# Kernel optimization log

Measured on AMD Instinct MI355X. Metric: run time of the kernel, lower is better.

The kernel has to match this reference:

```python
import jax, jax.numpy as jnp
import numpy as np

D_MODEL = 1024
NUM_HEADS = 16
DEPTH = D_MODEL // NUM_HEADS
MAX_LEN = 5000


def _make_pe(d_model=D_MODEL, max_len=MAX_LEN):
    # Faithful to torch PositionalEncoding: pe shape [max_len, 1, d_model]
    position = np.arange(max_len, dtype=np.float32)[:, None]
    div_term = np.exp(np.arange(0, d_model, 2, dtype=np.float32) * (-np.log(10000.0) / d_model))
    pe = np.zeros((max_len, d_model), dtype=np.float32)
    pe[:, 0::2] = np.sin(position * div_term)
    pe[:, 1::2] = np.cos(position * div_term)
    return jnp.asarray(pe[:, None, :])  # [max_len, 1, d_model]


def setup_inputs() -> dict:
    key = jax.random.key(0)
    ks = jax.random.split(key, 11)
    B, S, D = 4, 2048, D_MODEL
    s = 1.0 / np.sqrt(D)
    inp = {
        "v": jax.random.normal(ks[0], (B, S, D), jnp.float32),
        "k": jax.random.normal(ks[1], (B, S, D), jnp.float32),
        "q": jax.random.normal(ks[2], (B, S, D), jnp.float32),
        "wq_w": jax.random.normal(ks[3], (D, D), jnp.float32) * s,
        "wq_b": jnp.zeros((D,), jnp.float32),
        "wk_w": jax.random.normal(ks[4], (D, D), jnp.float32) * s,
        "wk_b": jnp.zeros((D,), jnp.float32),
        "wv_w": jax.random.normal(ks[5], (D, D), jnp.float32) * s,
        "wv_b": jnp.zeros((D,), jnp.float32),
        "dense_w": jax.random.normal(ks[6], (D, D), jnp.float32) * s,
        "dense_b": jnp.zeros((D,), jnp.float32),
        "pe": _make_pe(),
    }
    return inp


def _split_heads(x, B):
    # [B, S, D] -> [B, H, S, depth]
    return x.reshape(B, -1, NUM_HEADS, DEPTH).transpose(0, 2, 1, 3)


def reference(v, k, q, wq_w, wq_b, wk_w, wk_b, wv_w, wv_b, dense_w, dense_b, pe):
    B = q.shape[0]
    # Faithful bug-reproduction: pe[:batch] has shape [B, 1, D], broadcast over seq.
    pe_b = pe[:B]  # [B, 1, D]
    q = q + pe_b
    k = k + pe_b
    v = v + pe_b
    # Linear layers (torch: x @ W.T + b)
    qh = _split_heads(q @ wq_w.T + wq_b, B)  # [B,H,Sq,d]
    kh = _split_heads(k @ wk_w.T + wk_b, B)  # [B,H,Sk,d]
    vh = _split_heads(v @ wv_w.T + wv_b, B)  # [B,H,Sk,d]
    scale = 1.0 / jnp.sqrt(jnp.float32(DEPTH))
    logits = jnp.einsum("bhqd,bhkd->bhqk", qh, kh) * scale
    attn = jax.nn.softmax(logits, axis=-1)
    out = jnp.einsum("bhqk,bhkd->bhqd", attn, vh)
    out = out.transpose(0, 2, 1, 3).reshape(B, -1, D_MODEL)
    return out @ dense_w.T + dense_b
```

## Files before the change

### kernel.cpp

```cpp
#include <hip/hip_runtime.h>
#include <hip/hip_bf16.h>

typedef short short8 __attribute__((ext_vector_type(8)));
typedef float f32x4 __attribute__((ext_vector_type(4)));
typedef float f32x16 __attribute__((ext_vector_type(16)));
typedef unsigned int uint4v __attribute__((ext_vector_type(4)));

#define MFMA16(a, b, c) __builtin_amdgcn_mfma_f32_16x16x32_bf16(a, b, c, 0, 0, 0)
#define MFMA32(a, b, c) __builtin_amdgcn_mfma_f32_32x32x16_bf16(a, b, c, 0, 0, 0)

typedef __attribute__((address_space(1))) const unsigned int gas_u32;
typedef __attribute__((address_space(3))) unsigned int las_u32;

__device__ inline void gll16(const void* g, void* l) {
    __builtin_amdgcn_global_load_lds((gas_u32*)g, (las_u32*)l, 16, 0, 0);
}

__device__ inline unsigned short f2bf(float f) {
    unsigned u = __builtin_bit_cast(unsigned, f);
    u += 0x7fff + ((u >> 16) & 1);
    return (unsigned short)(u >> 16);
}

__device__ inline unsigned pk_perm(float a, float b, unsigned sel) {
    unsigned r;
    asm("v_perm_b32 %0, %1, %2, %3"
        : "=v"(r)
        : "v"(__builtin_bit_cast(unsigned, b)), "v"(__builtin_bit_cast(unsigned, a)), "s"(sel));
    return r;
}

__device__ inline float exp2_fast(float x) {
#if __has_builtin(__builtin_amdgcn_exp2f)
    return __builtin_amdgcn_exp2f(x);
#else
    float r; asm("v_exp_f32 %0, %1" : "=v"(r) : "v"(x)); return r;
#endif
}

__device__ inline void pl32_swap(unsigned &a, unsigned &b) {
    asm volatile("v_permlane32_swap_b32 %0, %1" : "+v"(a), "+v"(b));
}

__global__ void pe_cast3(const float* __restrict__ q, const float* __restrict__ k,
                         const float* __restrict__ v, const float* __restrict__ pe,
                         unsigned short* __restrict__ oq, unsigned short* __restrict__ ok,
                         unsigned short* __restrict__ ov) {
    const float* x = (blockIdx.y == 0) ? q : (blockIdx.y == 1) ? k : v;
    unsigned short* o = (blockIdx.y == 0) ? oq : (blockIdx.y == 1) ? ok : ov;
    int i = blockIdx.x * 256 + threadIdx.x;
    long e = (long)i * 4;
    int b = (int)(e >> 21);
    int d = (int)(e & 1023);
    float4 xv = reinterpret_cast<const float4*>(x)[i];
    float4 pv = *reinterpret_cast<const float4*>(pe + b * 1024 + d);
    ushort4 r;
    r.x = f2bf(xv.x + pv.x); r.y = f2bf(xv.y + pv.y);
    r.z = f2bf(xv.z + pv.z); r.w = f2bf(xv.w + pv.w);
    reinterpret_cast<ushort4*>(o)[i] = r;
}

__global__ void wcast4(const float* __restrict__ w0, const float* __restrict__ w1,
                       const float* __restrict__ w2, const float* __restrict__ w3,
                       unsigned short* __restrict__ o0) {
    const float* w = (blockIdx.y == 0) ? w0 : (blockIdx.y == 1) ? w1
                   : (blockIdx.y == 2) ? w2 : w3;
    unsigned short* o = o0 + (size_t)blockIdx.y * 1024 * 1024;
    int i = blockIdx.x * 256 + threadIdx.x;
    float4 xv = reinterpret_cast<const float4*>(w)[i];
    ushort4 r;
    r.x = f2bf(xv.x); r.y = f2bf(xv.y); r.z = f2bf(xv.z); r.w = f2bf(xv.w);
    reinterpret_cast<ushort4*>(o)[i] = r;
}

template <int MODE>
__global__ __launch_bounds__(256, 3) void gemm3(const unsigned short* __restrict__ A0,
                                                const unsigned short* __restrict__ W0,
                                                const float* __restrict__ bq,
                                                const float* __restrict__ bk,
                                                const float* __restrict__ bv,
                                                void* __restrict__ oq,
                                                void* __restrict__ ok,
                                                void* __restrict__ ov,
                                                float qscale) {
    const int NT = 32;
    __shared__ unsigned short lsA[3][128 * 32];
    __shared__ unsigned short lsB[3][128 * 32];

    int z = (MODE == 3) ? blockIdx.z : 0;
    const unsigned short* A = A0 + (size_t)z * 8192 * 1024;
    const unsigned short* W = W0 + (size_t)z * 1024 * 1024;
    const float* bias = (MODE == 3) ? ((z == 0) ? bq : (z == 1) ? bk : bv) : bq;
    float scale = (MODE == 3 && z == 0) ? qscale : 1.0f;

    int tid = threadIdx.x;
    int wave = tid >> 6, lane = tid & 63, lg = lane >> 4, l15 = lane & 15;
    int brow = blockIdx.x * 128;
    int bcol = blockIdx.y * 128;
    int wr = wave >> 1, wc = wave & 1;

    int c0 = wave * 64 + lane, c1 = 256 + c0;
    const unsigned short* sA0 = A + (long)(brow + (c0 >> 2)) * 1024 + ((c0 ^ (c0 >> 2)) & 3) * 8;
    const unsigned short* sA1 = A + (long)(brow + (c1 >> 2)) * 1024 + ((c1 ^ (c1 >> 2)) & 3) * 8;
    const unsigned short* sB0 = W + (long)(bcol + (c0 >> 2)) * 1024 + ((c0 ^ (c0 >> 2)) & 3) * 8;
    const unsigned short* sB1 = W + (long)(bcol + (c1 >> 2)) * 1024 + ((c1 ^ (c1 >> 2)) & 3) * 8;

    int cread = (lg * 16) ^ ((l15 & 3) << 4);

    f32x4 zero4 = {0.f, 0.f, 0.f, 0.f};
    f32x4 acc[4][4];
#pragma unroll
    for (int m = 0; m < 4; ++m)
#pragma unroll
        for (int n = 0; n < 4; ++n) acc[m][n] = zero4;

#define STG(k0, bi) do {                                                  \
        gll16(sA0 + (k0), (char*)lsA[bi] + (wave * 64) * 16);             \
        gll16(sA1 + (k0), (char*)lsA[bi] + (256 + wave * 64) * 16);       \
        gll16(sB0 + (k0), (char*)lsB[bi] + (wave * 64) * 16);             \
        gll16(sB1 + (k0), (char*)lsB[bi] + (256 + wave * 64) * 16);       \
    } while (0)

    STG(0, 0);
    STG(32, 1);

    int bi = 0, sb = 2;
    for (int t = 0; t < NT; ++t) {
        if (t == NT - 1) { asm volatile("s_waitcnt vmcnt(0)" ::: "memory"); }
        else             { asm volatile("s_waitcnt vmcnt(4)" ::: "memory"); }
        __builtin_amdgcn_s_barrier();
        if (t < NT - 2) STG((t + 2) * 32, sb);

        const char* KA = (const char*)lsA[bi];
        const char* KB = (const char*)lsB[bi];
        short8 af[4], bf_[4];
#pragma unroll
        for (int m = 0; m < 4; ++m) {
            int row = wr * 64 + m * 16 + l15;
            af[m] = *(const short8*)(KA + row * 64 + cread);
        }
#pragma unroll
        for (int n = 0; n < 4; ++n) {
            int col = wc * 64 + n * 16 + l15;
            bf_[n] = *(const short8*)(KB + col * 64 + cread);
        }
        __builtin_amdgcn_s_setprio(1);
#pragma unroll
        for (int m = 0; m < 4; ++m)
#pragma unroll
            for (int n = 0; n < 4; ++n) acc[m][n] = MFMA16(af[m], bf_[n], acc[m][n]);
        __builtin_amdgcn_s_setprio(0);

        bi = (bi == 2) ? 0 : bi + 1;
        sb = (sb == 2) ? 0 : sb + 1;
    }
#undef STG

    void* out = (MODE == 3) ? ((z == 0) ? oq : (z == 1) ? ok : ov) : oq;
#pragma unroll
    for (int m = 0; m < 4; ++m)
#pragma unroll
        for (int n = 0; n < 4; ++n) {
            int col = bcol + wc * 64 + n * 16 + l15;
            float bv_ = bias[col];
#pragma unroll
            for (int r = 0; r < 4; ++r) {
                int row = brow + wr * 64 + m * 16 + lg * 4 + r;
                float v = (acc[m][n][r] + bv_) * scale;
                if (MODE == 1) {
                    ((float*)out)[(long)row * 1024 + col] = v;
                } else {
                    int b = row >> 11, s = row & 2047;
                    if (z < 2) {
                        int h = col >> 6, d = col & 63;
                        ((unsigned short*)out)[(((long)(b * 16 + h) * 2048 + s) * 64 + d)] = f2bf(v);
                    } else {
                        ((unsigned short*)out)[((long)(b * 1024 + col)) * 2048 + s] = f2bf(v);
                    }
                }
            }
        }
}

__global__ __launch_bounds__(256, 2) void attn_kernel(const unsigned short* __restrict__ Qh,
                                                      const unsigned short* __restrict__ Kh,
                                                      const unsigned short* __restrict__ Vt,
                                                      unsigned short* __restrict__ Om) {
    const int S = 2048;
    const int NT = S / 64;
    int flat = blockIdx.x;
    int nf_ = (flat & 7) * 64 + (flat >> 3);
    int qt = nf_ & 7;
    int bh = nf_ >> 3;
    int b = bh >> 4, h = bh & 15;

    int tid = threadIdx.x, wave = tid >> 6, lane = tid & 63;
    int l31 = lane & 31, hi = lane >> 5;

    __shared__ __align__(16) unsigned short Kl[3][4096];
    __shared__ __align__(16) unsigned short Vtl[3][4096];

    const unsigned short* Qb = Qh + (long)bh * S * 64;
    const unsigned short* Kb = Kh + (long)bh * S * 64;
    const unsigned short* Vb = Vt + (long)bh * 64 * S;

    int colS = ((((tid & 7) * 16) ^ (((tid >> 3) & 7) << 4)) >> 1);
    const unsigned short* srcK = Kb + (tid >> 3) * 64 + colS;
    const unsigned short* srcV = Vb + (tid >> 3) * 2048 + colS;

    short8 aq[2][4];
    {
        const unsigned short* qrow = Qb + (long)(qt * 256 + wave * 64 + l31) * 64 + hi * 8;
#pragma unroll
        for (int qf = 0; qf < 2; ++qf)
#pragma unroll
            for (int s = 0; s < 4; ++s)
                aq[qf][s] = *(const short8*)(qrow + qf * 32 * 64 + s * 16);
    }

    f32x16 oacc[2][2], lacc[2], z16;
#pragma unroll
    for (int r = 0; r < 16; ++r) {
        oacc[0][0][r] = 0.f; oacc[0][1][r] = 0.f;
        oacc[1][0][r] = 0.f; oacc[1][1][r] = 0.f;
        lacc[0][r] = 0.f; lacc[1][r] = 0.f;
        z16[r] = 0.f;
    }

    const short8 ones8 = {0x3F80, 0x3F80, 0x3F80, 0x3F80, 0x3F80, 0x3F80, 0x3F80, 0x3F80};
    const unsigned SEL = 0x07060302u;

    int rb0 = l31 * 128;
    int swz = (l31 & 7) << 4;

#define STAGE(kt, bi) do {                                              \
        const unsigned short* sk = srcK + (kt) * 4096;                  \
        gll16(sk,         (char*)Kl[bi] + wave * 1024);                 \
        gll16(sk + 2048,  (char*)Kl[bi] + 4096 + wave * 1024);          \
        const unsigned short* sv = srcV + (kt) * 64;                    \
        gll16(sv,         (char*)Vtl[bi] + wave * 1024);                \
        gll16(sv + 65536, (char*)Vtl[bi] + 4096 + wave * 1024);         \
    } while (0)

    STAGE(0, 0);
    STAGE(1, 1);

    int bi = 0, sb = 2;
    for (int kt = 0; kt < NT; ++kt) {
        if (kt == NT - 1) { asm volatile("s_waitcnt vmcnt(0)" ::: "memory"); }
        else              { asm volatile("s_waitcnt vmcnt(4)" ::: "memory"); }
        __builtin_amdgcn_s_barrier();
        if (kt < NT - 2) STAGE(kt + 2, sb);

        const char* KlC = (const char*)Kl[bi];
        const char* VlC = (const char*)Vtl[bi];

        f32x16 sacc[2][2];
        __builtin_amdgcn_s_setprio(1);
#pragma unroll
        for (int blk = 0; blk < 2; ++blk) {
            short8 kf0 = *(const short8*)(KlC + blk * 4096 + rb0 + ((16 * hi) ^ swz));
            sacc[0][blk] = MFMA32(kf0, aq[0][0], z16);
            sacc[1][blk] = MFMA32(kf0, aq[1][0], z16);
#pragma unroll
            for (int s = 1; s < 4; ++s) {
                short8 kf = *(const short8*)(KlC + blk * 4096 + rb0 + ((32 * s + 16 * hi) ^ swz));
                sacc[0][blk] = MFMA32(kf, aq[0][s], sacc[0][blk]);
                sacc[1][blk] = MFMA32(kf, aq[1][s], sacc[1][blk]);
            }
        }
        __builtin_amdgcn_s_setprio(0);

#pragma unroll
        for (int qf = 0; qf < 2; ++qf)
#pragma unroll
            for (int blk = 0; blk < 2; ++blk)
#pragma unroll
                for (int r = 0; r < 16; ++r) sacc[qf][blk][r] = exp2_fast(sacc[qf][blk][r]);

#pragma unroll
        for (int s = 0; s < 4; ++s) {
            const int blk = s >> 1, base = (s & 1) * 8;
            short8 pa[2];
#pragma unroll
            for (int qf = 0; qf < 2; ++qf) {
                unsigned q0 = pk_perm(sacc[qf][blk][base + 0], sacc[qf][blk][base + 1], SEL);
                unsigned q1 = pk_perm(sacc[qf][blk][base + 2], sacc[qf][blk][base + 3], SEL);
                unsigned q2 = pk_perm(sacc[qf][blk][base + 4], sacc[qf][blk][base + 5], SEL);
                unsigned q3 = pk_perm(sacc[qf][blk][base + 6], sacc[qf][blk][base + 7], SEL);
                pl32_swap(q0, q2);
                pl32_swap(q1, q3);
                uint4v pw; pw[0] = q0; pw[1] = q1; pw[2] = q2; pw[3] = q3;
                pa[qf] = __builtin_bit_cast(short8, pw);
            }
            __builtin_amdgcn_s_setprio(1);
#pragma unroll
            for (int dblk = 0; dblk < 2; ++dblk) {
                short8 vf = *(const short8*)(VlC + dblk * 4096 + rb0 + ((32 * s + 16 * hi) ^ swz));
                oacc[0][dblk] = MFMA32(pa[0], vf, oacc[0][dblk]);
                oacc[1][dblk] = MFMA32(pa[1], vf, oacc[1][dblk]);
            }
            lacc[0] = MFMA32(pa[0], ones8, lacc[0]);
            lacc[1] = MFMA32(pa[1], ones8, lacc[1]);
            __builtin_amdgcn_s_setprio(0);
        }
        bi = (bi == 2) ? 0 : bi + 1;
        sb = (sb == 2) ? 0 : sb + 1;
    }
#undef STAGE

#pragma unroll
    for (int qf = 0; qf < 2; ++qf) {
        float inv[16];
#pragma unroll
        for (int r = 0; r < 16; ++r) inv[r] = 1.0f / lacc[qf][r];
        int qrow0 = qt * 256 + wave * 64 + qf * 32 + 4 * hi;
#pragma unroll
        for (int dblk = 0; dblk < 2; ++dblk)
#pragma unroll
            for (int r = 0; r < 16; ++r) {
                int qrow = qrow0 + (r & 3) + 8 * (r >> 2);
                int d = h * 64 + dblk * 32 + l31;
                float v = oacc[qf][dblk][r] * inv[r];
                Om[((long)b * 2048 + qrow) * 1024 + d] = f2bf(v);
            }
    }
}

extern "C" void kernel_launch(void* const* d_in, const int* in_sizes, int n_in,
                              void* d_out, int out_size, void* d_ws, size_t ws_size,
                              hipStream_t stream) {
    const float* v_in = (const float*)d_in[0];
    const float* k_in = (const float*)d_in[1];
    const float* q_in = (const float*)d_in[2];
    const float* wq_w = (const float*)d_in[3];
    const float* wq_b = (const float*)d_in[4];
    const float* wk_w = (const float*)d_in[5];
    const float* wk_b = (const float*)d_in[6];
    const float* wv_w = (const float*)d_in[7];
    const float* wv_b = (const float*)d_in[8];
    const float* wd_w = (const float*)d_in[9];
    const float* wd_b = (const float*)d_in[10];
    const float* pe   = (const float*)d_in[11];

    const long SZ = 8192L * 1024 * 2;
    char* ws = (char*)d_ws;
    unsigned short* xq = (unsigned short*)(ws + 0);
    unsigned short* xk = (unsigned short*)(ws + SZ);
    unsigned short* xv = (unsigned short*)(ws + 2 * SZ);
    unsigned short* qh = (unsigned short*)(ws + 3 * SZ);
    unsigned short* kh = (unsigned short*)(ws + 4 * SZ);
    unsigned short* vt = (unsigned short*)(ws + 5 * SZ);
    unsigned short* wqb16 = (unsigned short*)(ws + 6 * SZ);

    pe_cast3<<<dim3(8192, 3), 256, 0, stream>>>(q_in, k_in, v_in, pe, xq, xk, xv);
    wcast4<<<dim3(1024, 4), 256, 0, stream>>>(wq_w, wk_w, wv_w, wd_w, wqb16);

    const float QSCALE = 0.125f * 1.44269504088896f;
    gemm3<3><<<dim3(64, 8, 3), 256, 0, stream>>>(
        xq, wqb16, wq_b, wk_b, wv_b, qh, kh, vt, QSCALE);

    unsigned short* om = xq;
    attn_kernel<<<512, 256, 0, stream>>>(qh, kh, vt, om);

    gemm3<1><<<dim3(64, 8, 1), 256, 0, stream>>>(
        om, wqb16 + 3L * 1024 * 1024, wd_b, nullptr, nullptr, d_out, nullptr, nullptr, 1.0f);
}
```

Before: 217.5 us.

## Enlarge GEMM tiles to 256x256 with 512-thread blocks and BK=64 double buffering

Replaces the 128x128x32 triple-buffered projection GEMM with a templated kernel using 512 threads, 256-wide output tiles (256 or 128 rows), a K-step of 64 and two LDS buffers. Loads for the next stage are interleaved between MFMA groups. The V-transposed epilogue is vectorized to ushort4 stores. The aim is more operand reuse per LDS byte and fewer global loads per FLOP. In exchange it uses more registers and LDS, launches fewer blocks (384 and 256), and syncs with a full vmcnt(0) plus barrier on every iteration, which may reduce latency hiding.

```diff
diff --git a/kernel.cpp b/kernel.cpp
--- a/kernel.cpp
+++ b/kernel.cpp
@@ -73,8 +73,8 @@
     reinterpret_cast<ushort4*>(o)[i] = r;
 }
 
-template <int MODE>
-__global__ __launch_bounds__(256, 3) void gemm3(const unsigned short* __restrict__ A0,
+template <int MF, int MODE>
+__global__ __launch_bounds__(512, 2) void gemm4(const unsigned short* __restrict__ A0,
                                                 const unsigned short* __restrict__ W0,
                                                 const float* __restrict__ bq,
                                                 const float* __restrict__ bk,
@@ -83,9 +83,11 @@
                                                 void* __restrict__ ok,
                                                 void* __restrict__ ov,
                                                 float qscale) {
-    const int NT = 32;
-    __shared__ unsigned short lsA[3][128 * 32];
-    __shared__ unsigned short lsB[3][128 * 32];
+    const int NT = 16;
+    const int BM = MF * 32;
+    constexpr int AR = BM / 64;
+    __shared__ __align__(16) unsigned short lsA[2][BM * 64];
+    __shared__ __align__(16) unsigned short lsB[2][256 * 64];
 
     int z = (MODE == 3) ? blockIdx.z : 0;
     const unsigned short* A = A0 + (size_t)z * 8192 * 1024;
@@ -93,89 +95,153 @@
     const float* bias = (MODE == 3) ? ((z == 0) ? bq : (z == 1) ? bk : bv) : bq;
     float scale = (MODE == 3 && z == 0) ? qscale : 1.0f;
 
-    int tid = threadIdx.x;
-    int wave = tid >> 6, lane = tid & 63, lg = lane >> 4, l15 = lane & 15;
-    int brow = blockIdx.x * 128;
-    int bcol = blockIdx.y * 128;
-    int wr = wave >> 1, wc = wave & 1;
-
-    int c0 = wave * 64 + lane, c1 = 256 + c0;
-    const unsigned short* sA0 = A + (long)(brow + (c0 >> 2)) * 1024 + ((c0 ^ (c0 >> 2)) & 3) * 8;
-    const unsigned short* sA1 = A + (long)(brow + (c1 >> 2)) * 1024 + ((c1 ^ (c1 >> 2)) & 3) * 8;
-    const unsigned short* sB0 = W + (long)(bcol + (c0 >> 2)) * 1024 + ((c0 ^ (c0 >> 2)) & 3) * 8;
-    const unsigned short* sB1 = W + (long)(bcol + (c1 >> 2)) * 1024 + ((c1 ^ (c1 >> 2)) & 3) * 8;
-
-    int cread = (lg * 16) ^ ((l15 & 3) << 4);
-
-    f32x4 zero4 = {0.f, 0.f, 0.f, 0.f};
-    f32x4 acc[4][4];
-#pragma unroll
-    for (int m = 0; m < 4; ++m)
-#pragma unroll
-        for (int n = 0; n < 4; ++n) acc[m][n] = zero4;
-
-#define STG(k0, bi) do {                                                  \
-        gll16(sA0 + (k0), (char*)lsA[bi] + (wave * 64) * 16);             \
-        gll16(sA1 + (k0), (char*)lsA[bi] + (256 + wave * 64) * 16);       \
-        gll16(sB0 + (k0), (char*)lsB[bi] + (wave * 64) * 16);             \
-        gll16(sB1 + (k0), (char*)lsB[bi] + (256 + wave * 64) * 16);       \
+    int tid = threadIdx.x, wave = tid >> 6, lane = tid & 63;
+    int lg = lane >> 4, l15 = lane & 15;
+    int wr = wave >> 2, wc = wave & 3;
+    int brow = blockIdx.x * BM;
+    int bcol = blockIdx.y * 256;
+
+    int srow = tid >> 3;
+    int scol = ((tid ^ srow) & 7) * 8;
+    const unsigned short* pA = A + (long)(brow + srow) * 1024 + scol;
+    const unsigned short* pB = W + (long)(bcol + srow) * 1024 + scol;
+
+    f32x4 acc[MF][4];
+#pragma unroll
+    for (int m = 0; m < MF; ++m)
+#pragma unroll
+        for (int n = 0; n < 4; ++n) acc[m][n] = f32x4{0.f, 0.f, 0.f, 0.f};
+
+#define STG_A(t, bi) do {                                                   \
+        _Pragma("unroll")                                                   \
+        for (int j = 0; j < AR; ++j)                                        \
+            gll16(pA + (t) * 64 + j * 65536,                                \
+                  (char*)lsA[bi] + (j * 512 + wave * 64) * 16);             \
     } while (0)
-
-    STG(0, 0);
-    STG(32, 1);
-
-    int bi = 0, sb = 2;
+#define STG_B(t, bi) do {                                                   \
+        _Pragma("unroll")                                                   \
+        for (int j = 0; j < 4; ++j)                                         \
+            gll16(pB + (t) * 64 + j * 65536,                                \
+                  (char*)lsB[bi] + (j * 512 + wave * 64) * 16);             \
+    } while (0)
+
+    STG_A(0, 0);
+    STG_B(0, 0);
+    asm volatile("s_waitcnt vmcnt(0)" ::: "memory");
+    __syncthreads();
+
+    int swz = (l15 & 7) << 4;
     for (int t = 0; t < NT; ++t) {
-        if (t == NT - 1) { asm volatile("s_waitcnt vmcnt(0)" ::: "memory"); }
-        else             { asm volatile("s_waitcnt vmcnt(4)" ::: "memory"); }
-        __builtin_amdgcn_s_barrier();
-        if (t < NT - 2) STG((t + 2) * 32, sb);
-
-        const char* KA = (const char*)lsA[bi];
-        const char* KB = (const char*)lsB[bi];
-        short8 af[4], bf_[4];
-#pragma unroll
-        for (int m = 0; m < 4; ++m) {
-            int row = wr * 64 + m * 16 + l15;
-            af[m] = *(const short8*)(KA + row * 64 + cread);
+        int cb = t & 1;
+        const char* KA = (const char*)lsA[cb];
+        const char* KB = (const char*)lsB[cb];
+
+        if (t < NT - 1) STG_A(t + 1, cb ^ 1);
+
+        short8 af0[4][2], bf0[2][2];
+#pragma unroll
+        for (int m = 0; m < 4; ++m)
+#pragma unroll
+            for (int kk = 0; kk < 2; ++kk) {
+                int row = wr * (MF * 16) + m * 16 + l15;
+                af0[m][kk] = *(const short8*)(KA + row * 128 + (((kk * 4 + lg) << 4) ^ swz));
+            }
+#pragma unroll
+        for (int n = 0; n < 2; ++n)
+#pragma unroll
+            for (int kk = 0; kk < 2; ++kk) {
+                int row = wc * 64 + n * 16 + l15;
+                bf0[n][kk] = *(const short8*)(KB + row * 128 + (((kk * 4 + lg) << 4) ^ swz));
+            }
+        __builtin_amdgcn_s_setprio(1);
+#pragma unroll
+        for (int m = 0; m < 4; ++m)
+#pragma unroll
+            for (int n = 0; n < 2; ++n)
+#pragma unroll
+                for (int kk = 0; kk < 2; ++kk)
+                    acc[m][n] = MFMA16(af0[m][kk], bf0[n][kk], acc[m][n]);
+        __builtin_amdgcn_s_setprio(0);
+
+        if (t < NT - 1) STG_B(t + 1, cb ^ 1);
+
+        short8 bf1[2][2];
+#pragma unroll
+        for (int n = 0; n < 2; ++n)
+#pragma unroll
+            for (int kk = 0; kk < 2; ++kk) {
+                int row = wc * 64 + (n + 2) * 16 + l15;
+                bf1[n][kk] = *(const short8*)(KB + row * 128 + (((kk * 4 + lg) << 4) ^ swz));
+            }
+        __builtin_amdgcn_s_setprio(1);
+#pragma unroll
+        for (int m = 0; m < 4; ++m)
+#pragma unroll
+            for (int n = 0; n < 2; ++n)
+#pragma unroll
+                for (int kk = 0; kk < 2; ++kk)
+                    acc[m][n + 2] = MFMA16(af0[m][kk], bf1[n][kk], acc[m][n + 2]);
+        __builtin_amdgcn_s_setprio(0);
+
+        if (MF == 8) {
+            short8 af1[4][2];
+#pragma unroll
+            for (int m = 0; m < 4; ++m)
+#pragma unroll
+                for (int kk = 0; kk < 2; ++kk) {
+                    int row = wr * (MF * 16) + (m + 4) * 16 + l15;
+                    af1[m][kk] = *(const short8*)(KA + row * 128 + (((kk * 4 + lg) << 4) ^ swz));
+                }
+            __builtin_amdgcn_s_setprio(1);
+#pragma unroll
+            for (int m = 0; m < 4; ++m)
+#pragma unroll
+                for (int n = 0; n < 2; ++n)
+#pragma unroll
+                    for (int kk = 0; kk < 2; ++kk)
+                        acc[m + 4][n] = MFMA16(af1[m][kk], bf0[n][kk], acc[m + 4][n]);
+#pragma unroll
+            for (int m = 0; m < 4; ++m)
+#pragma unroll
+                for (int n = 0; n < 2; ++n)
+#pragma unroll
+                    for (int kk = 0; kk < 2; ++kk)
+                        acc[m + 4][n + 2] = MFMA16(af1[m][kk], bf1[n][kk], acc[m + 4][n + 2]);
+            __builtin_amdgcn_s_setprio(0);
         }
-#pragma unroll
-        for (int n = 0; n < 4; ++n) {
-            int col = wc * 64 + n * 16 + l15;
-            bf_[n] = *(const short8*)(KB + col * 64 + cread);
-        }
-        __builtin_amdgcn_s_setprio(1);
-#pragma unroll
-        for (int m = 0; m < 4; ++m)
-#pragma unroll
-            for (int n = 0; n < 4; ++n) acc[m][n] = MFMA16(af[m], bf_[n], acc[m][n]);
-        __builtin_amdgcn_s_setprio(0);
-
-        bi = (bi == 2) ? 0 : bi + 1;
-        sb = (sb == 2) ? 0 : sb + 1;
+
+        asm volatile("s_waitcnt vmcnt(0)" ::: "memory");
+        __syncthreads();
     }
-#undef STG
+#undef STG_A
+#undef STG_B
 
     void* out = (MODE == 3) ? ((z == 0) ? oq : (z == 1) ? ok : ov) : oq;
 #pragma unroll
-    for (int m = 0; m < 4; ++m)
+    for (int m = 0; m < MF; ++m)
 #pragma unroll
         for (int n = 0; n < 4; ++n) {
             int col = bcol + wc * 64 + n * 16 + l15;
             float bv_ = bias[col];
-#pragma unroll
-            for (int r = 0; r < 4; ++r) {
-                int row = brow + wr * 64 + m * 16 + lg * 4 + r;
-                float v = (acc[m][n][r] + bv_) * scale;
-                if (MODE == 1) {
-                    ((float*)out)[(long)row * 1024 + col] = v;
-                } else {
-                    int b = row >> 11, s = row & 2047;
-                    if (z < 2) {
-                        int h = col >> 6, d = col & 63;
+            int row0 = brow + wr * (MF * 16) + m * 16 + lg * 4;
+            if (MODE == 3 && z == 2) {
+                int b = row0 >> 11, s0 = row0 & 2047;
+                ushort4 pk;
+                pk.x = f2bf(acc[m][n][0] + bv_);
+                pk.y = f2bf(acc[m][n][1] + bv_);
+                pk.z = f2bf(acc[m][n][2] + bv_);
+                pk.w = f2bf(acc[m][n][3] + bv_);
+                *(ushort4*)((unsigned short*)out + ((long)(b * 1024 + col)) * 2048 + s0) = pk;
+            } else {
+#pragma unroll
+                for (int r = 0; r < 4; ++r) {
+                    int row = row0 + r;
+                    float v = (acc[m][n][r] + bv_) * scale;
+                    if (MODE == 1) {
+                        ((float*)out)[(long)row * 1024 + col] = v;
+                    } else {
+                        int b = row >> 11, s = row & 2047, h = col >> 6, d = col & 63;
                         ((unsigned short*)out)[(((long)(b * 16 + h) * 2048 + s) * 64 + d)] = f2bf(v);
-                    } else {
-                        ((unsigned short*)out)[((long)(b * 1024 + col)) * 2048 + s] = f2bf(v);
                     }
                 }
             }
@@ -357,12 +423,12 @@
     wcast4<<<dim3(1024, 4), 256, 0, stream>>>(wq_w, wk_w, wv_w, wd_w, wqb16);
 
     const float QSCALE = 0.125f * 1.44269504088896f;
-    gemm3<3><<<dim3(64, 8, 3), 256, 0, stream>>>(
+    gemm4<8, 3><<<dim3(32, 4, 3), 512, 0, stream>>>(
         xq, wqb16, wq_b, wk_b, wv_b, qh, kh, vt, QSCALE);
 
     unsigned short* om = xq;
     attn_kernel<<<512, 256, 0, stream>>>(qh, kh, vt, om);
 
-    gemm3<1><<<dim3(64, 8, 1), 256, 0, stream>>>(
+    gemm4<4, 1><<<dim3(64, 4, 1), 512, 0, stream>>>(
         om, wqb16 + 3L * 1024 * 1024, wd_b, nullptr, nullptr, d_out, nullptr, nullptr, 1.0f);
 }
```

After: 217.0 us. About the same (-0.2%).
